# Optimization experiments

Measured on AMD Instinct MI355X. Metric: run time of the kernel, lower is better.

The kernel has to match this reference:

```python
import jax, jax.numpy as jnp
import numpy as np

B, C1, C2, H, L, D, NC = 32, 256, 256, 64, 40, 768, 8
SIGMA_W = 0.1
EMB = (D + NC * 2) // 2  # 392


def _conv(x, w, scale, shift, pad):
    # ultralytics-style Conv: conv2d(bias=False) + eval-mode BN (folded into per-channel
    # scale/shift) + SiLU activation
    y = jax.lax.conv_general_dilated(x, w, (1, 1), [(pad, pad), (pad, pad)],
                                     dimension_numbers=('NCHW', 'OIHW', 'NCHW'))
    y = y * scale[None, :, None, None] + shift[None, :, None, None]
    return y * jax.nn.sigmoid(y)  # SiLU


def _l2norm(x, eps=1e-12):
    n = jnp.sqrt(jnp.sum(x * x, axis=1, keepdims=True))
    return x / jnp.maximum(n, eps)


def setup_inputs() -> dict:
    key = jax.random.key(0)
    ks = jax.random.split(key, 20)
    img = jax.random.normal(ks[0], (B, C1, H, H), jnp.float32)
    flang = jax.random.normal(ks[1], (B, L, D), jnp.float32)
    # contiguous valid mask with >=3 tokens (CLS + >=1 word + SEP)
    lens = jax.random.randint(ks[2], (B,), 3, L + 1)
    word_mask = (jnp.arange(L)[None, :] < lens[:, None]).astype(jnp.int32)
    p = lambda k, s: jax.random.normal(k, s, jnp.float32) * 0.02
    return {
        'img': img, 'flang': flang, 'word_mask': word_mask,
        'w_visu': p(ks[3], (C2, C1, 1, 1)), 's_visu': jnp.ones((C2,)), 'b_visu': jnp.zeros((C2,)),
        'w_g': p(ks[4], (NC, NC, 1, 1)), 's_g': jnp.ones((NC,)), 'b_g': jnp.zeros((NC,)),
        'w_b': p(ks[5], (NC, NC, 1, 1)), 's_b': jnp.ones((NC,)), 'b_b': jnp.zeros((NC,)),
        'W1': p(ks[6], (EMB, D)), 'b1': jnp.zeros((EMB,)),
        'W2': p(ks[7], (2 * NC, EMB)), 'b2': jnp.zeros((2 * NC,)),
        'w_f1': p(ks[8], (C1, C1, 1, 1)), 's_f1': jnp.ones((C1,)), 'b_f1': jnp.zeros((C1,)),
        'w_f2': p(ks[9], (C1, C1, 3, 3)), 's_f2': jnp.ones((C1,)), 'b_f2': jnp.zeros((C1,)),
        'w_f3': p(ks[10], (C2, C1, 1, 1)), 'bias_f3': jnp.zeros((C2,)),
        'add_weight': jnp.zeros((), jnp.float32),
    }


def reference(img, flang, word_mask, w_visu, s_visu, b_visu, w_g, s_g, b_g,
              w_b, s_b, b_b, W1, b1, W2, b2, w_f1, s_f1, b_f1, w_f2, s_f2, b_f2,
              w_f3, bias_f3, add_weight):
    height = img.shape[2]
    # mapping_visu: Conv 1x1 + BN + SiLU, then tanh
    map_visu = jnp.tanh(_conv(img, w_visu, s_visu, b_visu, 0))  # [B,C2,H,H]

    # vectorized get_avg_flang: mean over selected tokens excluding first and last selected
    m = word_mask.astype(jnp.int32)
    csum = jnp.cumsum(m, axis=1)                     # [B,L]
    total = csum[:, -1:]
    inner = ((m == 1) & (csum > 1) & (csum < total)).astype(flang.dtype)  # [B,L]
    cnt = jnp.sum(inner, axis=1, keepdims=True)
    flang_avg = jnp.sum(flang * inner[:, :, None], axis=1) / cnt  # [B,D]

    # mapping_lang: two stacked Linears (no activation between), then sigmoid
    h = flang_avg @ W1.T + b1
    map_flang = jax.nn.sigmoid(h @ W2.T + b2)        # [B,2*NC]
    maps = map_flang.reshape(-1, NC, 2)

    sigma = SIGMA_W * height
    yc = (maps[:, :, 0] * height).astype(jnp.int32)[:, :, None, None]
    xc = (maps[:, :, 1] * height).astype(jnp.int32)[:, :, None, None]
    gy, gx = jnp.meshgrid(jnp.arange(height), jnp.arange(height), indexing='ij')
    gy = gy[None, None]; gx = gx[None, None]
    d2 = ((gy - yc) ** 2 + (gx - xc) ** 2).astype(jnp.float32)
    weights = jnp.exp(-d2 / (2.0 * sigma ** 2))      # [B,NC,H,H]

    gamma = jnp.tanh(_conv(weights, w_g, s_g, b_g, 0))
    beta = jnp.tanh(_conv(weights, w_b, s_b, b_b, 0))
    g = jnp.mean(gamma, axis=1, keepdims=True)       # [B,1,H,H]
    b = jnp.max(beta, axis=1, keepdims=True)         # [B,1,H,H]

    v_film = _l2norm(g * map_visu + b)               # [B,C2,H,H]
    # mapping_fusion: Conv1x1 -> Conv3x3 -> plain Conv2d 1x1 with bias
    v = _conv(v_film, w_f1, s_f1, b_f1, 0)
    v = _conv(v, w_f2, s_f2, b_f2, 1)
    v_film = jax.lax.conv_general_dilated(v, w_f3, (1, 1), [(0, 0), (0, 0)],
                                          dimension_numbers=('NCHW', 'OIHW', 'NCHW'))
    v_film = v_film + bias_f3[None, :, None, None]

    add_w = jnp.tanh(add_weight)
    v_add = (1.0 + add_w) * img + (1.0 - add_w) * v_film
    return _l2norm(v_add)
```

## Files before the change

kernel.cpp:

```cpp
#include <hip/hip_runtime.h>
#include <hip/hip_bf16.h>

#define B_   32
#define C_   256
#define HH   64
#define P_   4096
#define L_   40
#define D_   768
#define NC_  8
#define EMB_ 392
#define CP_  (C_*P_)
#define LOS  264

typedef __attribute__((ext_vector_type(8))) short bf16x8;
typedef __attribute__((ext_vector_type(4))) float f32x4;
typedef unsigned short u16;

static __device__ __forceinline__ float silu_fast(float y) {
    return __fdividef(y, 1.f + __expf(-y));
}
static __device__ __forceinline__ float tanh_fast(float x) {
    return 1.f - __fdividef(2.f, __expf(2.f * x) + 1.f);
}
static __device__ __forceinline__ u16 f2b(float f) {
    __hip_bfloat16 h = __float2bfloat16(f);
    return *reinterpret_cast<u16*>(&h);
}
static __device__ __forceinline__ float b2f(u16 u) {
    unsigned v = ((unsigned)u) << 16;
    return __int_as_float((int)v);
}

typedef __attribute__((address_space(1))) const unsigned int g_u32;
typedef __attribute__((address_space(3))) unsigned int l_u32;
static __device__ __forceinline__ void gl_lds(const u16* g, short* l) {
    __builtin_amdgcn_global_load_lds((g_u32*)g, (l_u32*)l, 16, 0, 0);
}
#define VMCNT6() asm volatile("s_waitcnt vmcnt(6)" ::: "memory")
#define VMCNT4() asm volatile("s_waitcnt vmcnt(4)" ::: "memory")
#define VMCNT0() asm volatile("s_waitcnt vmcnt(0)" ::: "memory")
#define RBAR()  do { __builtin_amdgcn_s_barrier(); __builtin_amdgcn_sched_barrier(0); } while (0)

__global__ __launch_bounds__(256) void k_prep(
    const float* __restrict__ wv, const float* __restrict__ wf1,
    const float* __restrict__ wf3, const float* __restrict__ wf2,
    u16* __restrict__ WV, u16* __restrict__ WF1,
    u16* __restrict__ WF3, u16* __restrict__ WF2, u16* __restrict__ zbig)
{
    int i = blockIdx.x * 256 + threadIdx.x;
    int oc = i >> 8, ic = i & 255;
    WV[i]  = f2b(wv[i]);
    WF1[i] = f2b(wf1[i]);
    WF3[i] = f2b(wf3[i]);
#pragma unroll
    for (int tap = 0; tap < 9; ++tap)
        WF2[oc * 2304 + tap * 256 + ic] = f2b(wf2[oc * 2304 + ic * 9 + tap]);
    if (blockIdx.x == 0) {
        for (int z = threadIdx.x; z < 1024; z += 256) zbig[z] = 0;
    }
}

__global__ __launch_bounds__(256) void k_imgT(
    const float* __restrict__ img, u16* __restrict__ imgT)
{
    int b = blockIdx.z, pix0 = blockIdx.x * 32, ic0 = blockIdx.y * 32;
    int t = threadIdx.x;
    __shared__ float T[32][33];
    int ic = t >> 3, ps = (t & 7) * 4;
    f32x4 v = *(const f32x4*)&img[((size_t)b * C_ + ic0 + ic) * P_ + pix0 + ps];
    T[ic][ps] = v[0]; T[ic][ps + 1] = v[1]; T[ic][ps + 2] = v[2]; T[ic][ps + 3] = v[3];
    __syncthreads();
    int px = t >> 3, sg = (t & 7) * 4;
    u16 o0 = f2b(T[sg + 0][px]), o1 = f2b(T[sg + 1][px]);
    u16 o2 = f2b(T[sg + 2][px]), o3 = f2b(T[sg + 3][px]);
    uint2 val;
    val.x = (unsigned)o0 | ((unsigned)o1 << 16);
    val.y = (unsigned)o2 | ((unsigned)o3 << 16);
    *(uint2*)(imgT + ((size_t)b * P_ + pix0 + px) * C_ + ic0 + sg) = val;
}

__global__ __launch_bounds__(256) void k_lang(
    const float* __restrict__ flang, const int* __restrict__ wmask,
    const float* __restrict__ W1, const float* __restrict__ b1,
    const float* __restrict__ W2, const float* __restrict__ b2,
    int* __restrict__ centers)
{
    int b = blockIdx.x, tid = threadIdx.x;
    __shared__ float inner[L_];
    __shared__ float cnt_s;
    __shared__ float favg[D_];
    __shared__ float hbuf[EMB_];
    __shared__ float mfs[16];

    if (tid == 0) {
        int total = 0;
        for (int l = 0; l < L_; ++l) total += wmask[b * L_ + l];
        int c = 0, cntv = 0;
        for (int l = 0; l < L_; ++l) {
            int m = wmask[b * L_ + l];
            c += m;
            float f = (m == 1 && c > 1 && c < total) ? 1.f : 0.f;
            inner[l] = f;
            cntv += (f != 0.f);
        }
        cnt_s = (float)cntv;
    }
    __syncthreads();
    float cinv = 1.f / cnt_s;
    for (int d = tid; d < D_; d += 256) {
        float s = 0.f;
        for (int l = 0; l < L_; ++l)
            s += flang[((size_t)b * L_ + l) * D_ + d] * inner[l];
        favg[d] = s * cinv;
    }
    __syncthreads();
    for (int e = tid; e < EMB_; e += 256) {
        float s = b1[e];
        const float* w = W1 + (size_t)e * D_;
        for (int d = 0; d < D_; ++d) s += w[d] * favg[d];
        hbuf[e] = s;
    }
    __syncthreads();
    if (tid < 16) {
        float s = b2[tid];
        const float* w = W2 + tid * EMB_;
        for (int d = 0; d < EMB_; ++d) s += w[d] * hbuf[d];
        mfs[tid] = 1.f / (1.f + expf(-s));
    }
    __syncthreads();
    if (tid < NC_) {
        centers[b * (NC_ * 2) + tid * 2 + 0] = (int)(mfs[tid * 2 + 0] * (float)HH);
        centers[b * (NC_ * 2) + tid * 2 + 1] = (int)(mfs[tid * 2 + 1] * (float)HH);
    }
}

__global__ __launch_bounds__(256) void k_gb(
    const int* __restrict__ centers,
    const float* __restrict__ wg, const float* __restrict__ sg, const float* __restrict__ bg,
    const float* __restrict__ wb, const float* __restrict__ sb, const float* __restrict__ bb,
    float* __restrict__ gmap, float* __restrict__ bmap)
{
    int idx = blockIdx.x * 256 + threadIdx.x;
    int b = idx >> 12;
    int p = idx & 4095;
    int gy = p >> 6, gx = p & 63;

    float w[NC_];
#pragma unroll
    for (int nc = 0; nc < NC_; ++nc) {
        int yc = centers[b * (NC_ * 2) + nc * 2 + 0];
        int xc = centers[b * (NC_ * 2) + nc * 2 + 1];
        int dy = gy - yc, dx = gx - xc;
        w[nc] = __expf(-(float)(dy * dy + dx * dx) / 81.92f);
    }
    float gsum = 0.f, bmx = -1e30f;
#pragma unroll
    for (int c = 0; c < NC_; ++c) {
        float ag = 0.f, ab = 0.f;
#pragma unroll
        for (int ic = 0; ic < NC_; ++ic) {
            ag += wg[c * NC_ + ic] * w[ic];
            ab += wb[c * NC_ + ic] * w[ic];
        }
        gsum += tanh_fast(silu_fast(sg[c] * ag + bg[c]));
        bmx = fmaxf(bmx, tanh_fast(silu_fast(sb[c] * ab + bb[c])));
    }
    gmap[idx] = gsum * (1.f / (float)NC_);
    bmap[idx] = bmx;
}

static __device__ __forceinline__ void frag_load(const short* sA, const short* sW,
                                                 int l15, int qa, int w,
                                                 bf16x8 a[8], bf16x8 bb[4])
{
#pragma unroll
    for (int m = 0; m < 8; ++m)
        a[m] = *(const bf16x8*)&sA[(m * 16 + l15) * 32 + qa * 8];
#pragma unroll
    for (int n = 0; n < 4; ++n)
        bb[n] = *(const bf16x8*)&sW[(w * 64 + n * 16 + l15) * 32 + qa * 8];
}
static __device__ __forceinline__ void frag_compute(const bf16x8 a[8], const bf16x8 bb[4],
                                                    f32x4 acc[8][4])
{
#pragma unroll
    for (int m = 0; m < 8; ++m)
#pragma unroll
        for (int n = 0; n < 4; ++n)
            acc[m][n] = __builtin_amdgcn_mfma_f32_16x16x32_bf16(a[m], bb[n], acc[m][n], 0, 0, 0);
}

__global__ __launch_bounds__(256, 2) void k_visu(
    const u16* __restrict__ X, const u16* __restrict__ W,
    const float* __restrict__ s_visu, const float* __restrict__ b_visu,
    const float* __restrict__ gmap, const float* __restrict__ bmap,
    u16* __restrict__ Y)
{
    int b = blockIdx.y, p0 = blockIdx.x * 128, t = threadIdx.x;
    int lane = t & 63, w = t >> 6;
    int l15 = t & 15, q = (t >> 4) & 3;
    int qa = q ^ ((l15 >> 1) & 3);
    int lc = (lane & 3) ^ ((lane >> 3) & 3);
    int lp = lane >> 2;
    __shared__ __align__(16) short SM[3 * 12288];
    __shared__ float red[4][128];
    __shared__ float invs[128];
    const u16* Xb = X + (size_t)b * CP_;

    f32x4 acc[8][4];
#pragma unroll
    for (int m = 0; m < 8; ++m)
#pragma unroll
        for (int n = 0; n < 4; ++n) acc[m][n] = (f32x4)0.f;

    auto stage = [&](int s, int buf) {
        int k0 = s * 32;
        short* bA = SM + buf * 12288;
        short* bW = bA + 4096;
#pragma unroll
        for (int i = 0; i < 2; ++i) {
            int pr = (w * 2 + i) * 16 + lp;
            gl_lds(Xb + (size_t)(p0 + pr) * C_ + k0 + lc * 8, bA + (w * 2 + i) * 512);
        }
#pragma unroll
        for (int j = 0; j < 4; ++j) {
            int oc = (w * 4 + j) * 16 + lp;
            gl_lds(W + (size_t)oc * 256 + k0 + lc * 8, bW + (w * 4 + j) * 512);
        }
    };

    stage(0, 0);
    stage(1, 1);
    VMCNT6();
    RBAR();
    int cur = 0;
    for (int s = 0; s < 8; ++s) {
        const short* bA = SM + cur * 12288;
        bf16x8 a[8], bb[4];
        frag_load(bA, bA + 4096, l15, qa, w, a, bb);
        if (s < 6) stage(s + 2, (cur == 0) ? 2 : cur - 1);
        frag_compute(a, bb, acc);
        if (s < 6) { VMCNT6(); } else { VMCNT0(); }
        RBAR();
        cur = (cur == 2) ? 0 : cur + 1;
    }

    float sc[4], sh[4];
#pragma unroll
    for (int n = 0; n < 4; ++n) {
        int oc = w * 64 + n * 16 + l15;
        sc[n] = s_visu[oc]; sh[n] = b_visu[oc];
    }
    short* LO = SM;
#pragma unroll
    for (int m = 0; m < 8; ++m) {
        f32x4 gv = *(const f32x4*)&gmap[(size_t)b * P_ + p0 + m * 16 + q * 4];
        f32x4 bm = *(const f32x4*)&bmap[(size_t)b * P_ + p0 + m * 16 + q * 4];
        float ps[4] = {0.f, 0.f, 0.f, 0.f};
#pragma unroll
        for (int n = 0; n < 4; ++n)
#pragma unroll
            for (int r = 0; r < 4; ++r) {
                float y = sc[n] * acc[m][n][r] + sh[n];
                float v = gv[r] * tanh_fast(silu_fast(y)) + bm[r];
                ps[r] += v * v;
                LO[(m * 16 + q * 4 + r) * LOS + w * 64 + n * 16 + l15] = (short)f2b(v);
            }
#pragma unroll
        for (int r = 0; r < 4; ++r) {
            float p = ps[r];
            p += __shfl_xor(p, 1);
            p += __shfl_xor(p, 2);
            p += __shfl_xor(p, 4);
            p += __shfl_xor(p, 8);
            if (l15 == 0) red[w][m * 16 + q * 4 + r] = p;
        }
    }
    __syncthreads();
    if (t < 128) {
        float s = red[0][t] + red[1][t] + red[2][t] + red[3][t];
        invs[t] = 1.f / fmaxf(sqrtf(s), 1e-12f);
    }
    __syncthreads();

    u16* Yb = Y + (size_t)b * CP_ + (size_t)p0 * C_;
#pragma unroll
    for (int h = 0; h < 2; ++h) {
        int row = h * 64 + (t >> 2);
        float inv = invs[row];
        const short* sp = &LO[row * LOS];
        u16* dp = Yb + (size_t)row * C_;
#pragma unroll
        for (int u = 0; u < 8; ++u) {
            int c = (t & 3) * 8 + u * 32;
            uint4 vv = *(const uint4*)(sp + c);
            const u16* e = (const u16*)&vv;
            uint4 o;
            u16* oe = (u16*)&o;
#pragma unroll
            for (int k = 0; k < 8; ++k) oe[k] = f2b(b2f(e[k]) * inv);
            *(uint4*)(dp + c) = o;
        }
    }
}

__global__ __launch_bounds__(256, 2) void k_f1(
    const u16* __restrict__ X, const u16* __restrict__ W,
    const float* __restrict__ scale, const float* __restrict__ shift,
    u16* __restrict__ Y)
{
    int b = blockIdx.y, p0 = blockIdx.x * 128, t = threadIdx.x;
    int lane = t & 63, w = t >> 6;
    int l15 = t & 15, q = (t >> 4) & 3;
    int qa = q ^ ((l15 >> 1) & 3);
    int lc = (lane & 3) ^ ((lane >> 3) & 3);
    int lp = lane >> 2;
    __shared__ __align__(16) short SM[3 * 12288];
    const u16* Xb = X + (size_t)b * CP_;

    f32x4 acc[8][4];
#pragma unroll
    for (int m = 0; m < 8; ++m)
#pragma unroll
        for (int n = 0; n < 4; ++n) acc[m][n] = (f32x4)0.f;

    auto stage = [&](int s, int buf) {
        int k0 = s * 32;
        short* bA = SM + buf * 12288;
        short* bW = bA + 4096;
#pragma unroll
        for (int i = 0; i < 2; ++i) {
            int pr = (w * 2 + i) * 16 + lp;
            gl_lds(Xb + (size_t)(p0 + pr) * C_ + k0 + lc * 8, bA + (w * 2 + i) * 512);
        }
#pragma unroll
        for (int j = 0; j < 4; ++j) {
            int oc = (w * 4 + j) * 16 + lp;
            gl_lds(W + (size_t)oc * 256 + k0 + lc * 8, bW + (w * 4 + j) * 512);
        }
    };

    stage(0, 0);
    stage(1, 1);
    VMCNT6();
    RBAR();
    int cur = 0;
    for (int s = 0; s < 8; ++s) {
        const short* bA = SM + cur * 12288;
        bf16x8 a[8], bb[4];
        frag_load(bA, bA + 4096, l15, qa, w, a, bb);
        if (s < 6) stage(s + 2, (cur == 0) ? 2 : cur - 1);
        frag_compute(a, bb, acc);
        if (s < 6) { VMCNT6(); } else { VMCNT0(); }
        RBAR();
        cur = (cur == 2) ? 0 : cur + 1;
    }

    float sc[4], sh[4];
#pragma unroll
    for (int n = 0; n < 4; ++n) {
        int oc = w * 64 + n * 16 + l15;
        sc[n] = scale[oc]; sh[n] = shift[oc];
    }
    short* LO = SM;
#pragma unroll
    for (int m = 0; m < 8; ++m)
#pragma unroll
        for (int n = 0; n < 4; ++n)
#pragma unroll
            for (int r = 0; r < 4; ++r) {
                float v = silu_fast(sc[n] * acc[m][n][r] + sh[n]);
                LO[(m * 16 + q * 4 + r) * LOS + w * 64 + n * 16 + l15] = (short)f2b(v);
            }
    __syncthreads();

    u16* Yb = Y + (size_t)b * CP_ + (size_t)p0 * C_;
#pragma unroll
    for (int h = 0; h < 2; ++h) {
        int row = h * 64 + (t >> 2);
        const short* sp = &LO[row * LOS];
        u16* dp = Yb + (size_t)row * C_;
#pragma unroll
        for (int u = 0; u < 8; ++u) {
            int c = (t & 3) * 8 + u * 32;
            *(uint4*)(dp + c) = *(const uint4*)(sp + c);
        }
    }
}

__global__ __launch_bounds__(512, 1) void k_f2(
    const u16* __restrict__ X, const u16* __restrict__ W,
    const float* __restrict__ scale, const float* __restrict__ shift,
    const u16* __restrict__ zbig, u16* __restrict__ Y)
{
    int b = blockIdx.y, p0 = blockIdx.x * 256, t = threadIdx.x;
    int lane = t & 63, w = t >> 6;
    int wr = w >> 2, wc = w & 3;
    int l15 = t & 15, q = (t >> 4) & 3;
    int qa = q ^ ((l15 >> 1) & 3);
    int lc = (lane & 3) ^ ((lane >> 3) & 3);
    int lp = lane >> 2;
    __shared__ __align__(16) short SM[3 * 16384];
    const u16* Xb = X + (size_t)b * CP_;

    f32x4 acc[8][4];
#pragma unroll
    for (int m = 0; m < 8; ++m)
#pragma unroll
        for (int n = 0; n < 4; ++n) acc[m][n] = (f32x4)0.f;

    const u16* ap0 = zbig;
    const u16* ap1 = zbig;
    const u16* wp0 = W + (size_t)((w * 2 + 0) * 16 + lp) * 2304 + lc * 8;
    const u16* wp1 = W + (size_t)((w * 2 + 1) * 16 + lp) * 2304 + lc * 8;
    int ss = 0;

    auto stage_next = [&](int buf) {
        if ((ss & 7) == 0) {
            int tap = ss >> 3;
            int dy = tap / 3 - 1, dx = tap - (tap / 3) * 3 - 1;
            int pA = p0 + (w * 2 + 0) * 16 + lp;
            int y0 = (pA >> 6) + dy, x0 = (pA & 63) + dx;
            ap0 = ((unsigned)y0 < (unsigned)HH && (unsigned)x0 < (unsigned)HH)
                  ? Xb + (size_t)(y0 * HH + x0) * C_ + lc * 8 : zbig + lc * 8;
            int pB = p0 + (w * 2 + 1) * 16 + lp;
            int y1 = (pB >> 6) + dy, x1 = (pB & 63) + dx;
            ap1 = ((unsigned)y1 < (unsigned)HH && (unsigned)x1 < (unsigned)HH)
                  ? Xb + (size_t)(y1 * HH + x1) * C_ + lc * 8 : zbig + lc * 8;
        }
        short* bA = SM + buf * 16384;
        short* bW = bA + 8192;
        gl_lds(ap0, bA + (w * 2 + 0) * 512);
        gl_lds(ap1, bA + (w * 2 + 1) * 512);
        gl_lds(wp0, bW + (w * 2 + 0) * 512);
        gl_lds(wp1, bW + (w * 2 + 1) * 512);
        ap0 += 32; ap1 += 32;
        wp0 += 32; wp1 += 32;
        ++ss;
    };

    stage_next(0);
    stage_next(1);
    VMCNT4();
    RBAR();
    int cur = 0;
    for (int s = 0; s < 72; ++s) {
        const short* bA = SM + cur * 16384;
        const short* bW = bA + 8192;
        bf16x8 a[8], bb[4];
#pragma unroll
        for (int m = 0; m < 8; ++m)
            a[m] = *(const bf16x8*)&bA[(wr * 128 + m * 16 + l15) * 32 + qa * 8];
#pragma unroll
        for (int n = 0; n < 4; ++n)
            bb[n] = *(const bf16x8*)&bW[(wc * 64 + n * 16 + l15) * 32 + qa * 8];
        if (s < 70) {
            int nb = cur == 0 ? 2 : cur - 1;
            stage_next(nb);
        }
        frag_compute(a, bb, acc);
        if (s < 70) { VMCNT4(); } else { VMCNT0(); }
        RBAR();
        cur = cur == 2 ? 0 : cur + 1;
    }

    float sc[4], sh[4];
#pragma unroll
    for (int n = 0; n < 4; ++n) {
        int oc = wc * 64 + n * 16 + l15;
        sc[n] = scale[oc]; sh[n] = shift[oc];
    }
    short* LO = SM;
    u16* Yb = Y + (size_t)b * CP_ + (size_t)p0 * C_;
#pragma unroll
    for (int h = 0; h < 2; ++h) {
        __syncthreads();
        if (wr == h) {
#pragma unroll
            for (int m = 0; m < 8; ++m)
#pragma unroll
                for (int n = 0; n < 4; ++n)
#pragma unroll
                    for (int r = 0; r < 4; ++r) {
                        float v = silu_fast(sc[n] * acc[m][n][r] + sh[n]);
                        LO[(m * 16 + q * 4 + r) * LOS + wc * 64 + n * 16 + l15] = (short)f2b(v);
                    }
        }
        __syncthreads();
        {
            int row = t >> 2;
            const short* sp = &LO[row * LOS];
            u16* dp = Yb + (size_t)(h * 128 + row) * C_;
#pragma unroll
            for (int u = 0; u < 4; ++u) {
                int c = (t & 3) * 8 + u * 64;
                *(uint4*)(dp + c) = *(const uint4*)(sp + c);
                *(uint4*)(dp + c + 32) = *(const uint4*)(sp + c + 32);
            }
        }
    }
}

__global__ __launch_bounds__(256, 2) void k_final(
    const u16* __restrict__ X, const u16* __restrict__ W,
    const float* __restrict__ bias_f3, const float* __restrict__ img,
    const float* __restrict__ add_w, float* __restrict__ out)
{
    int b = blockIdx.y, p0 = blockIdx.x * 128, t = threadIdx.x;
    int lane = t & 63, w = t >> 6;
    int l15 = t & 15, q = (t >> 4) & 3;
    int qa = q ^ ((l15 >> 1) & 3);
    int lc = (lane & 3) ^ ((lane >> 3) & 3);
    int lp = lane >> 2;
    __shared__ __align__(16) short SM[3 * 12288];
    __shared__ float red[4][128];
    __shared__ float invs[128];
    const u16* Xb = X + (size_t)b * CP_;

    f32x4 acc[8][4];
#pragma unroll
    for (int m = 0; m < 8; ++m)
#pragma unroll
        for (int n = 0; n < 4; ++n) acc[m][n] = (f32x4)0.f;

    auto stage = [&](int s, int buf) {
        int k0 = s * 32;
        short* bA = SM + buf * 12288;
        short* bW = bA + 4096;
#pragma unroll
        for (int i = 0; i < 2; ++i) {
            int pr = (w * 2 + i) * 16 + lp;
            gl_lds(Xb + (size_t)(p0 + pr) * C_ + k0 + lc * 8, bA + (w * 2 + i) * 512);
        }
#pragma unroll
        for (int j = 0; j < 4; ++j) {
            int oc = (w * 4 + j) * 16 + lp;
            gl_lds(W + (size_t)oc * 256 + k0 + lc * 8, bW + (w * 4 + j) * 512);
        }
    };

    stage(0, 0);
    stage(1, 1);
    VMCNT6();
    RBAR();
    int cur = 0;
    for (int s = 0; s < 8; ++s) {
        const short* bA = SM + cur * 12288;
        bf16x8 a[8], bb[4];
        frag_load(bA, bA + 4096, l15, qa, w, a, bb);
        if (s < 6) stage(s + 2, (cur == 0) ? 2 : cur - 1);
        frag_compute(a, bb, acc);
        if (s < 6) { VMCNT6(); } else { VMCNT0(); }
        RBAR();
        cur = (cur == 2) ? 0 : cur + 1;
    }

    float aw = tanhf(add_w[0]);
    float c1 = 1.f + aw, c2 = 1.f - aw;
    float bf[4];
#pragma unroll
    for (int n = 0; n < 4; ++n) bf[n] = bias_f3[w * 64 + n * 16 + l15];

#pragma unroll
    for (int m = 0; m < 8; ++m) {
        float ps[4] = {0.f, 0.f, 0.f, 0.f};
#pragma unroll
        for (int n = 0; n < 4; ++n) {
            int oc = w * 64 + n * 16 + l15;
            f32x4 iv = *(const f32x4*)&img[((size_t)b * C_ + oc) * P_ + p0 + m * 16 + q * 4];
#pragma unroll
            for (int r = 0; r < 4; ++r) {
                float v = c1 * iv[r] + c2 * (acc[m][n][r] + bf[n]);
                acc[m][n][r] = v;
                ps[r] += v * v;
            }
        }
#pragma unroll
        for (int r = 0; r < 4; ++r) {
            float p = ps[r];
            p += __shfl_xor(p, 1);
            p += __shfl_xor(p, 2);
            p += __shfl_xor(p, 4);
            p += __shfl_xor(p, 8);
            if (l15 == 0) red[w][m * 16 + q * 4 + r] = p;
        }
    }
    __syncthreads();
    if (t < 128) {
        float s = red[0][t] + red[1][t] + red[2][t] + red[3][t];
        invs[t] = 1.f / fmaxf(sqrtf(s), 1e-12f);
    }
    __syncthreads();

    float* TP = (float*)SM;
#pragma unroll
    for (int cc = 0; cc < 2; ++cc) {
#pragma unroll
        for (int mm = 0; mm < 4; ++mm) {
            int m = cc * 4 + mm;
            f32x4 iv = *(const f32x4*)&invs[m * 16 + q * 4];
#pragma unroll
            for (int n = 0; n < 4; ++n) {
                int oc = w * 64 + n * 16 + l15;
                f32x4 o;
#pragma unroll
                for (int r = 0; r < 4; ++r) o[r] = acc[m][n][r] * iv[r];
                *(f32x4*)&TP[(size_t)oc * 68 + mm * 16 + q * 4] = o;
            }
        }
        __syncthreads();
        {
            int c16 = (t & 15) * 4;
#pragma unroll
            for (int u = 0; u < 16; ++u) {
                int row = u * 16 + (t >> 4);
                *(f32x4*)&out[((size_t)b * C_ + row) * P_ + p0 + cc * 64 + c16] =
                    *(const f32x4*)&TP[(size_t)row * 68 + c16];
            }
        }
        __syncthreads();
    }
}

extern "C" void kernel_launch(void* const* d_in, const int* in_sizes, int n_in,
                              void* d_out, int out_size, void* d_ws, size_t ws_size,
                              hipStream_t stream)
{
    const float* img     = (const float*)d_in[0];
    const float* flang   = (const float*)d_in[1];
    const int*   wmask   = (const int*)d_in[2];
    const float* w_visu  = (const float*)d_in[3];
    const float* s_visu  = (const float*)d_in[4];
    const float* b_visu  = (const float*)d_in[5];
    const float* w_g     = (const float*)d_in[6];
    const float* s_g     = (const float*)d_in[7];
    const float* b_g     = (const float*)d_in[8];
    const float* w_b     = (const float*)d_in[9];
    const float* s_b     = (const float*)d_in[10];
    const float* b_b     = (const float*)d_in[11];
    const float* W1      = (const float*)d_in[12];
    const float* b1      = (const float*)d_in[13];
    const float* W2      = (const float*)d_in[14];
    const float* b2      = (const float*)d_in[15];
    const float* w_f1    = (const float*)d_in[16];
    const float* s_f1    = (const float*)d_in[17];
    const float* b_f1    = (const float*)d_in[18];
    const float* w_f2    = (const float*)d_in[19];
    const float* s_f2    = (const float*)d_in[20];
    const float* b_f2    = (const float*)d_in[21];
    const float* w_f3    = (const float*)d_in[22];
    const float* bias_f3 = (const float*)d_in[23];
    const float* add_w   = (const float*)d_in[24];

    float* out = (float*)d_out;

    u16* bigA = (u16*)d_ws;
    u16* bigB = bigA + (size_t)B_ * CP_;
    u16* WV   = bigB + (size_t)B_ * CP_;
    u16* WF1  = WV + 65536;
    u16* WF3  = WF1 + 65536;
    u16* WF2  = WF3 + 65536;
    float* gmap = (float*)(WF2 + 589824);
    float* bmap = gmap + (size_t)B_ * P_;
    int* centers = (int*)(bmap + (size_t)B_ * P_);
    u16* zbig = (u16*)(centers + 512);

    k_prep<<<256, 256, 0, stream>>>(w_visu, w_f1, w_f3, w_f2, WV, WF1, WF3, WF2, zbig);
    k_lang<<<B_, 256, 0, stream>>>(flang, wmask, W1, b1, W2, b2, centers);
    k_gb<<<(B_ * P_) / 256, 256, 0, stream>>>(centers, w_g, s_g, b_g, w_b, s_b, b_b, gmap, bmap);
    k_imgT<<<dim3(P_ / 32, C_ / 32, B_), 256, 0, stream>>>(img, bigB);
    k_visu<<<dim3(P_ / 128, B_), 256, 0, stream>>>(bigB, WV, s_visu, b_visu, gmap, bmap, bigA);
    k_f1<<<dim3(P_ / 128, B_), 256, 0, stream>>>(bigA, WF1, s_f1, b_f1, bigB);
    k_f2<<<dim3(P_ / 256, B_), 512, 0, stream>>>(bigB, WF2, s_f2, b_f2, zbig, bigA);
    k_final<<<dim3(P_ / 128, B_), 256, 0, stream>>>(bigA, WF3, bias_f3, img, add_w, out);
}
```

Before: 435.2 us.

## Enlarge 1x1-conv GEMM tiles to 256 pixels with 512-thread blocks

The three 1x1-conv GEMM kernels (visu, f1, final) now use 256-pixel tiles and 512-thread blocks arranged as 2x4 waves instead of 128-pixel tiles with 256 threads. Each weight tile loaded into LDS is shared by twice as many pixels, so weight traffic per output drops. Epilogues are restructured to write through LDS in two halves. In exchange occupancy drops to one larger block per CU, LDS use grows, and there are extra barriers in the epilogue.

Measured after the change: 467.2 us. +7.3%, slower.

```diff
diff --git a/kernel.cpp b/kernel.cpp
--- a/kernel.cpp
+++ b/kernel.cpp
@@ -36,7 +36,6 @@
 static __device__ __forceinline__ void gl_lds(const u16* g, short* l) {
     __builtin_amdgcn_global_load_lds((g_u32*)g, (l_u32*)l, 16, 0, 0);
 }
-#define VMCNT6() asm volatile("s_waitcnt vmcnt(6)" ::: "memory")
 #define VMCNT4() asm volatile("s_waitcnt vmcnt(4)" ::: "memory")
 #define VMCNT0() asm volatile("s_waitcnt vmcnt(0)" ::: "memory")
 #define RBAR()  do { __builtin_amdgcn_s_barrier(); __builtin_amdgcn_sched_barrier(0); } while (0)
@@ -169,17 +168,6 @@
     bmap[idx] = bmx;
 }
 
-static __device__ __forceinline__ void frag_load(const short* sA, const short* sW,
-                                                 int l15, int qa, int w,
-                                                 bf16x8 a[8], bf16x8 bb[4])
-{
-#pragma unroll
-    for (int m = 0; m < 8; ++m)
-        a[m] = *(const bf16x8*)&sA[(m * 16 + l15) * 32 + qa * 8];
-#pragma unroll
-    for (int n = 0; n < 4; ++n)
-        bb[n] = *(const bf16x8*)&sW[(w * 64 + n * 16 + l15) * 32 + qa * 8];
-}
 static __device__ __forceinline__ void frag_compute(const bf16x8 a[8], const bf16x8 bb[4],
                                                     f32x4 acc[8][4])
 {
@@ -190,21 +178,22 @@
             acc[m][n] = __builtin_amdgcn_mfma_f32_16x16x32_bf16(a[m], bb[n], acc[m][n], 0, 0, 0);
 }
 
-__global__ __launch_bounds__(256, 2) void k_visu(
+__global__ __launch_bounds__(512, 1) void k_visu(
     const u16* __restrict__ X, const u16* __restrict__ W,
     const float* __restrict__ s_visu, const float* __restrict__ b_visu,
     const float* __restrict__ gmap, const float* __restrict__ bmap,
     u16* __restrict__ Y)
 {
-    int b = blockIdx.y, p0 = blockIdx.x * 128, t = threadIdx.x;
+    int b = blockIdx.y, p0 = blockIdx.x * 256, t = threadIdx.x;
     int lane = t & 63, w = t >> 6;
+    int wr = w >> 2, wc = w & 3;
     int l15 = t & 15, q = (t >> 4) & 3;
     int qa = q ^ ((l15 >> 1) & 3);
     int lc = (lane & 3) ^ ((lane >> 3) & 3);
     int lp = lane >> 2;
-    __shared__ __align__(16) short SM[3 * 12288];
-    __shared__ float red[4][128];
-    __shared__ float invs[128];
+    __shared__ __align__(16) short SM[3 * 16384];
+    __shared__ float red[4][256];
+    __shared__ float invs[256];
     const u16* Xb = X + (size_t)b * CP_;
 
     f32x4 acc[8][4];
@@ -215,32 +204,38 @@
 
     auto stage = [&](int s, int buf) {
         int k0 = s * 32;
-        short* bA = SM + buf * 12288;
-        short* bW = bA + 4096;
+        short* bA = SM + buf * 16384;
+        short* bW = bA + 8192;
 #pragma unroll
         for (int i = 0; i < 2; ++i) {
             int pr = (w * 2 + i) * 16 + lp;
             gl_lds(Xb + (size_t)(p0 + pr) * C_ + k0 + lc * 8, bA + (w * 2 + i) * 512);
         }
 #pragma unroll
-        for (int j = 0; j < 4; ++j) {
-            int oc = (w * 4 + j) * 16 + lp;
-            gl_lds(W + (size_t)oc * 256 + k0 + lc * 8, bW + (w * 4 + j) * 512);
+        for (int j = 0; j < 2; ++j) {
+            int oc = (w * 2 + j) * 16 + lp;
+            gl_lds(W + (size_t)oc * 256 + k0 + lc * 8, bW + (w * 2 + j) * 512);
         }
     };
 
     stage(0, 0);
     stage(1, 1);
-    VMCNT6();
+    VMCNT4();
     RBAR();
     int cur = 0;
     for (int s = 0; s < 8; ++s) {
-        const short* bA = SM + cur * 12288;
+        const short* bA = SM + cur * 16384;
+        const short* bW = bA + 8192;
         bf16x8 a[8], bb[4];
-        frag_load(bA, bA + 4096, l15, qa, w, a, bb);
+#pragma unroll
+        for (int m = 0; m < 8; ++m)
+            a[m] = *(const bf16x8*)&bA[(wr * 128 + m * 16 + l15) * 32 + qa * 8];
+#pragma unroll
+        for (int n = 0; n < 4; ++n)
+            bb[n] = *(const bf16x8*)&bW[(wc * 64 + n * 16 + l15) * 32 + qa * 8];
         if (s < 6) stage(s + 2, (cur == 0) ? 2 : cur - 1);
         frag_compute(a, bb, acc);
-        if (s < 6) { VMCNT6(); } else { VMCNT0(); }
+        if (s < 6) { VMCNT4(); } else { VMCNT0(); }
         RBAR();
         cur = (cur == 2) ? 0 : cur + 1;
     }
@@ -248,14 +243,14 @@
     float sc[4], sh[4];
 #pragma unroll
     for (int n = 0; n < 4; ++n) {
-        int oc = w * 64 + n * 16 + l15;
+        int oc = wc * 64 + n * 16 + l15;
         sc[n] = s_visu[oc]; sh[n] = b_visu[oc];
     }
-    short* LO = SM;
 #pragma unroll
     for (int m = 0; m < 8; ++m) {
-        f32x4 gv = *(const f32x4*)&gmap[(size_t)b * P_ + p0 + m * 16 + q * 4];
-        f32x4 bm = *(const f32x4*)&bmap[(size_t)b * P_ + p0 + m * 16 + q * 4];
+        int px = wr * 128 + m * 16 + q * 4;
+        f32x4 gv = *(const f32x4*)&gmap[(size_t)b * P_ + p0 + px];
+        f32x4 bm = *(const f32x4*)&bmap[(size_t)b * P_ + p0 + px];
         float ps[4] = {0.f, 0.f, 0.f, 0.f};
 #pragma unroll
         for (int n = 0; n < 4; ++n)
@@ -263,8 +258,8 @@
             for (int r = 0; r < 4; ++r) {
                 float y = sc[n] * acc[m][n][r] + sh[n];
                 float v = gv[r] * tanh_fast(silu_fast(y)) + bm[r];
+                acc[m][n][r] = v;
                 ps[r] += v * v;
-                LO[(m * 16 + q * 4 + r) * LOS + w * 64 + n * 16 + l15] = (short)f2b(v);
             }
 #pragma unroll
         for (int r = 0; r < 4; ++r) {
@@ -273,49 +268,62 @@
             p += __shfl_xor(p, 2);
             p += __shfl_xor(p, 4);
             p += __shfl_xor(p, 8);
-            if (l15 == 0) red[w][m * 16 + q * 4 + r] = p;
-        }
-    }
-    __syncthreads();
-    if (t < 128) {
+            if (l15 == 0) red[wc][px + r] = p;
+        }
+    }
+    __syncthreads();
+    if (t < 256) {
         float s = red[0][t] + red[1][t] + red[2][t] + red[3][t];
         invs[t] = 1.f / fmaxf(sqrtf(s), 1e-12f);
     }
     __syncthreads();
 
+    short* LO = SM;
     u16* Yb = Y + (size_t)b * CP_ + (size_t)p0 * C_;
 #pragma unroll
     for (int h = 0; h < 2; ++h) {
-        int row = h * 64 + (t >> 2);
-        float inv = invs[row];
-        const short* sp = &LO[row * LOS];
-        u16* dp = Yb + (size_t)row * C_;
-#pragma unroll
-        for (int u = 0; u < 8; ++u) {
-            int c = (t & 3) * 8 + u * 32;
-            uint4 vv = *(const uint4*)(sp + c);
-            const u16* e = (const u16*)&vv;
-            uint4 o;
-            u16* oe = (u16*)&o;
-#pragma unroll
-            for (int k = 0; k < 8; ++k) oe[k] = f2b(b2f(e[k]) * inv);
-            *(uint4*)(dp + c) = o;
-        }
-    }
-}
-
-__global__ __launch_bounds__(256, 2) void k_f1(
+        __syncthreads();
+        if (wr == h) {
+#pragma unroll
+            for (int m = 0; m < 8; ++m) {
+                int px = h * 128 + m * 16 + q * 4;
+                f32x4 iv = *(const f32x4*)&invs[px];
+#pragma unroll
+                for (int n = 0; n < 4; ++n)
+#pragma unroll
+                    for (int r = 0; r < 4; ++r)
+                        LO[(m * 16 + q * 4 + r) * LOS + wc * 64 + n * 16 + l15] =
+                            (short)f2b(acc[m][n][r] * iv[r]);
+            }
+        }
+        __syncthreads();
+        {
+            int row = t >> 2;
+            const short* sp = &LO[row * LOS];
+            u16* dp = Yb + (size_t)(h * 128 + row) * C_;
+#pragma unroll
+            for (int u = 0; u < 4; ++u) {
+                int c = (t & 3) * 8 + u * 64;
+                *(uint4*)(dp + c) = *(const uint4*)(sp + c);
+                *(uint4*)(dp + c + 32) = *(const uint4*)(sp + c + 32);
+            }
+        }
+    }
+}
+
+__global__ __launch_bounds__(512, 1) void k_f1(
     const u16* __restrict__ X, const u16* __restrict__ W,
     const float* __restrict__ scale, const float* __restrict__ shift,
     u16* __restrict__ Y)
 {
-    int b = blockIdx.y, p0 = blockIdx.x * 128, t = threadIdx.x;
+    int b = blockIdx.y, p0 = blockIdx.x * 256, t = threadIdx.x;
     int lane = t & 63, w = t >> 6;
+    int wr = w >> 2, wc = w & 3;
     int l15 = t & 15, q = (t >> 4) & 3;
     int qa = q ^ ((l15 >> 1) & 3);
     int lc = (lane & 3) ^ ((lane >> 3) & 3);
     int lp = lane >> 2;
-    __shared__ __align__(16) short SM[3 * 12288];
+    __shared__ __align__(16) short SM[3 * 16384];
     const u16* Xb = X + (size_t)b * CP_;
 
     f32x4 acc[8][4];
@@ -326,32 +334,38 @@
 
     auto stage = [&](int s, int buf) {
         int k0 = s * 32;
-        short* bA = SM + buf * 12288;
-        short* bW = bA + 4096;
+        short* bA = SM + buf * 16384;
+        short* bW = bA + 8192;
 #pragma unroll
         for (int i = 0; i < 2; ++i) {
             int pr = (w * 2 + i) * 16 + lp;
             gl_lds(Xb + (size_t)(p0 + pr) * C_ + k0 + lc * 8, bA + (w * 2 + i) * 512);
         }
 #pragma unroll
-        for (int j = 0; j < 4; ++j) {
-            int oc = (w * 4 + j) * 16 + lp;
-            gl_lds(W + (size_t)oc * 256 + k0 + lc * 8, bW + (w * 4 + j) * 512);
+        for (int j = 0; j < 2; ++j) {
+            int oc = (w * 2 + j) * 16 + lp;
+            gl_lds(W + (size_t)oc * 256 + k0 + lc * 8, bW + (w * 2 + j) * 512);
         }
     };
 
     stage(0, 0);
     stage(1, 1);
-    VMCNT6();
+    VMCNT4();
     RBAR();
     int cur = 0;
     for (int s = 0; s < 8; ++s) {
-        const short* bA = SM + cur * 12288;
+        const short* bA = SM + cur * 16384;
+        const short* bW = bA + 8192;
         bf16x8 a[8], bb[4];
-        frag_load(bA, bA + 4096, l15, qa, w, a, bb);
+#pragma unroll
+        for (int m = 0; m < 8; ++m)
+            a[m] = *(const bf16x8*)&bA[(wr * 128 + m * 16 + l15) * 32 + qa * 8];
+#pragma unroll
+        for (int n = 0; n < 4; ++n)
+            bb[n] = *(const bf16x8*)&bW[(wc * 64 + n * 16 + l15) * 32 + qa * 8];
         if (s < 6) stage(s + 2, (cur == 0) ? 2 : cur - 1);
         frag_compute(a, bb, acc);
-        if (s < 6) { VMCNT6(); } else { VMCNT0(); }
+        if (s < 6) { VMCNT4(); } else { VMCNT0(); }
         RBAR();
         cur = (cur == 2) ? 0 : cur + 1;
     }
@@ -359,31 +373,36 @@
     float sc[4], sh[4];
 #pragma unroll
     for (int n = 0; n < 4; ++n) {
-        int oc = w * 64 + n * 16 + l15;
+        int oc = wc * 64 + n * 16 + l15;
         sc[n] = scale[oc]; sh[n] = shift[oc];
     }
     short* LO = SM;
-#pragma unroll
-    for (int m = 0; m < 8; ++m)
-#pragma unroll
-        for (int n = 0; n < 4; ++n)
-#pragma unroll
-            for (int r = 0; r < 4; ++r) {
-                float v = silu_fast(sc[n] * acc[m][n][r] + sh[n]);
-                LO[(m * 16 + q * 4 + r) * LOS + w * 64 + n * 16 + l15] = (short)f2b(v);
+    u16* Yb = Y + (size_t)b * CP_ + (size_t)p0 * C_;
+#pragma unroll
+    for (int h = 0; h < 2; ++h) {
+        __syncthreads();
+        if (wr == h) {
+#pragma unroll
+            for (int m = 0; m < 8; ++m)
+#pragma unroll
+                for (int n = 0; n < 4; ++n)
+#pragma unroll
+                    for (int r = 0; r < 4; ++r) {
+                        float v = silu_fast(sc[n] * acc[m][n][r] + sh[n]);
+                        LO[(m * 16 + q * 4 + r) * LOS + wc * 64 + n * 16 + l15] = (short)f2b(v);
+                    }
+        }
+        __syncthreads();
+        {
+            int row = t >> 2;
+            const short* sp = &LO[row * LOS];
+            u16* dp = Yb + (size_t)(h * 128 + row) * C_;
+#pragma unroll
+            for (int u = 0; u < 4; ++u) {
+                int c = (t & 3) * 8 + u * 64;
+                *(uint4*)(dp + c) = *(const uint4*)(sp + c);
+                *(uint4*)(dp + c + 32) = *(const uint4*)(sp + c + 32);
             }
-    __syncthreads();
-
-    u16* Yb = Y + (size_t)b * CP_ + (size_t)p0 * C_;
-#pragma unroll
-    for (int h = 0; h < 2; ++h) {
-        int row = h * 64 + (t >> 2);
-        const short* sp = &LO[row * LOS];
-        u16* dp = Yb + (size_t)row * C_;
-#pragma unroll
-        for (int u = 0; u < 8; ++u) {
-            int c = (t & 3) * 8 + u * 32;
-            *(uint4*)(dp + c) = *(const uint4*)(sp + c);
         }
     }
 }
@@ -501,20 +520,21 @@
     }
 }
 
-__global__ __launch_bounds__(256, 2) void k_final(
+__global__ __launch_bounds__(512, 1) void k_final(
     const u16* __restrict__ X, const u16* __restrict__ W,
     const float* __restrict__ bias_f3, const float* __restrict__ img,
     const float* __restrict__ add_w, float* __restrict__ out)
 {
-    int b = blockIdx.y, p0 = blockIdx.x * 128, t = threadIdx.x;
+    int b = blockIdx.y, p0 = blockIdx.x * 256, t = threadIdx.x;
     int lane = t & 63, w = t >> 6;
+    int wr = w >> 2, wc = w & 3;
     int l15 = t & 15, q = (t >> 4) & 3;
     int qa = q ^ ((l15 >> 1) & 3);
     int lc = (lane & 3) ^ ((lane >> 3) & 3);
     int lp = lane >> 2;
-    __shared__ __align__(16) short SM[3 * 12288];
-    __shared__ float red[4][128];
-    __shared__ float invs[128];
+    __shared__ __align__(16) short SM[3 * 16384];
+    __shared__ float red[4][256];
+    __shared__ float invs[256];
     const u16* Xb = X + (size_t)b * CP_;
 
     f32x4 acc[8][4];
@@ -525,32 +545,38 @@
 
     auto stage = [&](int s, int buf) {
         int k0 = s * 32;
-        short* bA = SM + buf * 12288;
-        short* bW = bA + 4096;
+        short* bA = SM + buf * 16384;
+        short* bW = bA + 8192;
 #pragma unroll
         for (int i = 0; i < 2; ++i) {
             int pr = (w * 2 + i) * 16 + lp;
             gl_lds(Xb + (size_t)(p0 + pr) * C_ + k0 + lc * 8, bA + (w * 2 + i) * 512);
         }
 #pragma unroll
-        for (int j = 0; j < 4; ++j) {
-            int oc = (w * 4 + j) * 16 + lp;
-            gl_lds(W + (size_t)oc * 256 + k0 + lc * 8, bW + (w * 4 + j) * 512);
+        for (int j = 0; j < 2; ++j) {
+            int oc = (w * 2 + j) * 16 + lp;
+            gl_lds(W + (size_t)oc * 256 + k0 + lc * 8, bW + (w * 2 + j) * 512);
         }
     };
 
     stage(0, 0);
     stage(1, 1);
-    VMCNT6();
+    VMCNT4();
     RBAR();
     int cur = 0;
     for (int s = 0; s < 8; ++s) {
-        const short* bA = SM + cur * 12288;
+        const short* bA = SM + cur * 16384;
+        const short* bW = bA + 8192;
         bf16x8 a[8], bb[4];
-        frag_load(bA, bA + 4096, l15, qa, w, a, bb);
+#pragma unroll
+        for (int m = 0; m < 8; ++m)
+            a[m] = *(const bf16x8*)&bA[(wr * 128 + m * 16 + l15) * 32 + qa * 8];
+#pragma unroll
+        for (int n = 0; n < 4; ++n)
+            bb[n] = *(const bf16x8*)&bW[(wc * 64 + n * 16 + l15) * 32 + qa * 8];
         if (s < 6) stage(s + 2, (cur == 0) ? 2 : cur - 1);
         frag_compute(a, bb, acc);
-        if (s < 6) { VMCNT6(); } else { VMCNT0(); }
+        if (s < 6) { VMCNT4(); } else { VMCNT0(); }
         RBAR();
         cur = (cur == 2) ? 0 : cur + 1;
     }
@@ -559,15 +585,16 @@
     float c1 = 1.f + aw, c2 = 1.f - aw;
     float bf[4];
 #pragma unroll
-    for (int n = 0; n < 4; ++n) bf[n] = bias_f3[w * 64 + n * 16 + l15];
+    for (int n = 0; n < 4; ++n) bf[n] = bias_f3[wc * 64 + n * 16 + l15];
 
 #pragma unroll
     for (int m = 0; m < 8; ++m) {
+        int px = wr * 128 + m * 16 + q * 4;
         float ps[4] = {0.f, 0.f, 0.f, 0.f};
 #pragma unroll
         for (int n = 0; n < 4; ++n) {
-            int oc = w * 64 + n * 16 + l15;
-            f32x4 iv = *(const f32x4*)&img[((size_t)b * C_ + oc) * P_ + p0 + m * 16 + q * 4];
+            int oc = wc * 64 + n * 16 + l15;
+            f32x4 iv = *(const f32x4*)&img[((size_t)b * C_ + oc) * P_ + p0 + px];
 #pragma unroll
             for (int r = 0; r < 4; ++r) {
                 float v = c1 * iv[r] + c2 * (acc[m][n][r] + bf[n]);
@@ -582,11 +609,11 @@
             p += __shfl_xor(p, 2);
             p += __shfl_xor(p, 4);
             p += __shfl_xor(p, 8);
-            if (l15 == 0) red[w][m * 16 + q * 4 + r] = p;
-        }
-    }
-    __syncthreads();
-    if (t < 128) {
+            if (l15 == 0) red[wc][px + r] = p;
+        }
+    }
+    __syncthreads();
+    if (t < 256) {
         float s = red[0][t] + red[1][t] + red[2][t] + red[3][t];
         invs[t] = 1.f / fmaxf(sqrtf(s), 1e-12f);
     }
@@ -594,26 +621,29 @@
 
     float* TP = (float*)SM;
 #pragma unroll
-    for (int cc = 0; cc < 2; ++cc) {
-#pragma unroll
-        for (int mm = 0; mm < 4; ++mm) {
-            int m = cc * 4 + mm;
-            f32x4 iv = *(const f32x4*)&invs[m * 16 + q * 4];
-#pragma unroll
-            for (int n = 0; n < 4; ++n) {
-                int oc = w * 64 + n * 16 + l15;
-                f32x4 o;
-#pragma unroll
-                for (int r = 0; r < 4; ++r) o[r] = acc[m][n][r] * iv[r];
-                *(f32x4*)&TP[(size_t)oc * 68 + mm * 16 + q * 4] = o;
+    for (int cc = 0; cc < 4; ++cc) {
+        if (wr == (cc >> 1)) {
+#pragma unroll
+            for (int mm = 0; mm < 4; ++mm) {
+                int m = (cc & 1) * 4 + mm;
+                int px = wr * 128 + m * 16 + q * 4;
+                f32x4 iv = *(const f32x4*)&invs[px];
+#pragma unroll
+                for (int n = 0; n < 4; ++n) {
+                    int oc = wc * 64 + n * 16 + l15;
+                    f32x4 o;
+#pragma unroll
+                    for (int r = 0; r < 4; ++r) o[r] = acc[m][n][r] * iv[r];
+                    *(f32x4*)&TP[(size_t)oc * 68 + mm * 16 + q * 4] = o;
+                }
             }
         }
         __syncthreads();
         {
             int c16 = (t & 15) * 4;
 #pragma unroll
-            for (int u = 0; u < 16; ++u) {
-                int row = u * 16 + (t >> 4);
+            for (int u = 0; u < 8; ++u) {
+                int row = u * 32 + (t >> 4);
                 *(f32x4*)&out[((size_t)b * C_ + row) * P_ + p0 + cc * 64 + c16] =
                     *(const f32x4*)&TP[(size_t)row * 68 + c16];
             }
@@ -669,8 +699,8 @@
     k_lang<<<B_, 256, 0, stream>>>(flang, wmask, W1, b1, W2, b2, centers);
     k_gb<<<(B_ * P_) / 256, 256, 0, stream>>>(centers, w_g, s_g, b_g, w_b, s_b, b_b, gmap, bmap);
     k_imgT<<<dim3(P_ / 32, C_ / 32, B_), 256, 0, stream>>>(img, bigB);
-    k_visu<<<dim3(P_ / 128, B_), 256, 0, stream>>>(bigB, WV, s_visu, b_visu, gmap, bmap, bigA);
-    k_f1<<<dim3(P_ / 128, B_), 256, 0, stream>>>(bigA, WF1, s_f1, b_f1, bigB);
+    k_visu<<<dim3(P_ / 256, B_), 512, 0, stream>>>(bigB, WV, s_visu, b_visu, gmap, bmap, bigA);
+    k_f1<<<dim3(P_ / 256, B_), 512, 0, stream>>>(bigA, WF1, s_f1, b_f1, bigB);
     k_f2<<<dim3(P_ / 256, B_), 512, 0, stream>>>(bigB, WF2, s_f2, b_f2, zbig, bigA);
-    k_final<<<dim3(P_ / 128, B_), 256, 0, stream>>>(bigA, WF3, bias_f3, img, add_w, out);
-}
+    k_final<<<dim3(P_ / 256, B_), 512, 0, stream>>>(bigA, WF3, bias_f3, img, add_w, out);
+}
```
